# Kernel tuning notes

Hardware: AMD Instinct MI355X
Metric: run time of the kernel (lower is better)

## Reference

```python
import jax, jax.numpy as jnp
import numpy as np

DICE_TH = 0.4
CLS_TH = 0.5
LN_EPS = 1e-5


def setup_inputs() -> dict:
    key = jax.random.key(0)
    P, C, NC, K = 200_000, 256, 200, 24  # points, clicks, classes, latent prototypes
    ks = jax.random.split(key, 6)
    # structured masks: each click targets one of K prototype regions so the
    # dice/cls thresholds yield a non-degenerate grouping
    point_proto = jax.random.randint(ks[0], (P,), 0, K)
    proto_vals = jax.random.uniform(ks[1], (P,))
    click_proto = jax.random.randint(ks[2], (C,), 0, K)
    base = (point_proto[:, None] == click_proto[None, :]).astype(jnp.float32)  # [P, C]
    noise = jax.random.uniform(ks[3], (P, C))
    masks_heatmap = base * (0.6 + 0.4 * proto_vals[:, None]) + 0.02 * noise
    class_emb = jax.random.normal(ks[4], (K, NC)) * 3.0
    cls_logits = class_emb[click_proto] + 0.3 * jax.random.normal(ks[5], (C, NC))
    clicks_list = jax.random.randint(ks[0], (C,), 0, NC)  # unused (random_clicks=True)
    return {"masks_heatmap": masks_heatmap, "cls_logits": cls_logits,
            "clicks_list": clicks_list}


def _associate(masks_heatmap, cls_logits):
    """Greedy dice+cls-similarity grouping (random_clicks=True path).
    Returns labels[c] = leader click index of the group containing click c."""
    M = masks_heatmap                      # [P, C]
    C = M.shape[1]
    s = M.sum(0)                           # [C]
    # dice[i, j] = 2 * m_i . m_j / (sum(m_i) + sum(m_j))  (all pairs at once)
    dice = 2.0 * (M.T @ M) / (s[:, None] + s[None, :])
    # F.layer_norm over last dim, no affine
    mu = cls_logits.mean(-1, keepdims=True)
    var = ((cls_logits - mu) ** 2).mean(-1, keepdims=True)
    p = (cls_logits - mu) / jnp.sqrt(var + LN_EPS)
    sim = p @ p.T                          # [C, C]
    cond = (dice > DICE_TH) & (sim > CLS_TH)

    def step(carry, x):
        assigned, labels = carry
        i, row = x
        # skip if i already suppressed; take unsuppressed clicks matching row i
        take = row & (~assigned) & (~assigned[i])
        return (assigned | take, jnp.where(take, i, labels)), None

    init = (jnp.zeros((C,), bool), jnp.full((C,), -1, jnp.int32))
    (assigned, labels), _ = jax.lax.scan(
        step, init, (jnp.arange(C, dtype=jnp.int32), cond))
    return labels


def _merge(labels, masks_heatmap, cls_logits):
    """reduction='max': per-group max over member clicks. Unused group slots
    (non-leader indices) are zero-filled and flagged by group_valid."""
    C = masks_heatmap.shape[1]
    seg = jnp.where(labels >= 0, labels, C)  # route unassigned to dump segment
    counts = jax.ops.segment_sum(jnp.ones((C,), jnp.float32), seg,
                                 num_segments=C + 1)[:C]
    group_valid = counts > 0
    nm = jax.ops.segment_max(masks_heatmap.T, seg, num_segments=C + 1)[:C]  # [C, P]
    nc = jax.ops.segment_max(cls_logits, seg, num_segments=C + 1)[:C]      # [C, NC]
    new_masks = jnp.where(group_valid[:, None], nm, 0.0).T  # [P, C]
    new_cls = jnp.where(group_valid[:, None], nc, 0.0)      # [C, NC]
    return new_masks, new_cls, group_valid


def reference(masks_heatmap, cls_logits, clicks_list):
    labels = _associate(masks_heatmap, cls_logits)
    new_masks, new_cls, group_valid = _merge(labels, masks_heatmap, cls_logits)
    return labels, group_valid, new_masks, new_cls
```

## Files before the change

### kernel.cpp

```cpp
#include <hip/hip_runtime.h>
#include <cstdint>
#include <cstddef>

constexpr int P  = 200000;
constexpr int C  = 256;
constexpr int NC = 200;
#define DICE_TH 0.4f
#define CLS_TH  0.5f
#define LN_EPS  1e-5f

constexpr int KC = 1600;
constexpr int NCHUNK = 125;

constexpr size_t WS_G       = 0;
constexpr size_t WS_S       = 262144;
constexpr size_t WS_PROW    = 263168;
constexpr size_t WS_PT      = 467968;
constexpr size_t WS_COND    = 672768;
constexpr size_t WS_MSTART  = 680960;
constexpr size_t WS_MEMBERS = 682240;

typedef float floatx4 __attribute__((ext_vector_type(4)));
typedef float floatx16 __attribute__((ext_vector_type(16)));
typedef __bf16 bf16x4 __attribute__((ext_vector_type(4)));
typedef __bf16 bf16x8 __attribute__((ext_vector_type(8)));
typedef unsigned short ushort4v __attribute__((ext_vector_type(4)));
typedef unsigned short ushort8 __attribute__((ext_vector_type(8)));

constexpr int LDA = 40;

__global__ __launch_bounds__(256, 2) void gram_mfma_kernel(
    const float* __restrict__ M, float* __restrict__ G, float* __restrict__ s) {
  __shared__ unsigned short Abf[128 * LDA];
  __shared__ unsigned short Bbf[128 * LDA];
  __shared__ float scol[128];

  const int type = blockIdx.x;
  const int i0 = (type == 2) ? 128 : 0;
  const int j0 = (type == 0) ? 0 : 128;
  const bool diag = (type != 1);
  const int tid = threadIdx.x;
  const int wv = tid >> 6, lane = tid & 63;
  const int g  = tid & 31;
  const int kq = tid >> 5;
  const int k0 = blockIdx.y * KC;
  const int swz = (g & 3) << 1;

  if (tid < 128) scol[tid] = 0.f;

  floatx16 acc[4];
#pragma unroll
  for (int t = 0; t < 4; ++t)
#pragma unroll
    for (int r = 0; r < 16; ++r) acc[t][r] = 0.f;
  float ss[4] = {0.f, 0.f, 0.f, 0.f};

  const int mrow = lane & 31;
  const int kgrp = (lane >> 5) * 8;
  const int xa = ((mrow >> 2) & 3) << 1;
  const int wbase = (kq ^ swz) << 2;

  for (int step = 0; step < KC / 32; ++step) {
    const int kb = k0 + step * 32 + 4 * kq;
    {
      const float* src = M + (size_t)kb * 256 + i0 + 4 * g;
      floatx4 r0 = *reinterpret_cast<const floatx4*>(src);
      floatx4 r1 = *reinterpret_cast<const floatx4*>(src + 256);
      floatx4 r2 = *reinterpret_cast<const floatx4*>(src + 512);
      floatx4 r3 = *reinterpret_cast<const floatx4*>(src + 768);
      if (diag) {
        ss[0] += r0[0] + r1[0] + r2[0] + r3[0];
        ss[1] += r0[1] + r1[1] + r2[1] + r3[1];
        ss[2] += r0[2] + r1[2] + r2[2] + r3[2];
        ss[3] += r0[3] + r1[3] + r2[3] + r3[3];
      }
#pragma unroll
      for (int cc = 0; cc < 4; ++cc) {
        floatx4 f = {r0[cc], r1[cc], r2[cc], r3[cc]};
        bf16x4 b = __builtin_convertvector(f, bf16x4);
        *reinterpret_cast<ushort4v*>(&Abf[(4 * g + cc) * LDA + wbase]) =
            __builtin_bit_cast(ushort4v, b);
      }
    }
    if (!diag) {
      const float* src = M + (size_t)kb * 256 + j0 + 4 * g;
      floatx4 r0 = *reinterpret_cast<const floatx4*>(src);
      floatx4 r1 = *reinterpret_cast<const floatx4*>(src + 256);
      floatx4 r2 = *reinterpret_cast<const floatx4*>(src + 512);
      floatx4 r3 = *reinterpret_cast<const floatx4*>(src + 768);
#pragma unroll
      for (int cc = 0; cc < 4; ++cc) {
        floatx4 f = {r0[cc], r1[cc], r2[cc], r3[cc]};
        bf16x4 b = __builtin_convertvector(f, bf16x4);
        *reinterpret_cast<ushort4v*>(&Bbf[(4 * g + cc) * LDA + wbase]) =
            __builtin_bit_cast(ushort4v, b);
      }
    }
    __syncthreads();

    const unsigned short* Bsrc = diag ? Abf : Bbf;
#pragma unroll
    for (int sub = 0; sub < 2; ++sub) {
      const int ko = sub * 16 + kgrp;
      const int koff = (((ko >> 2) ^ xa) << 2);
      bf16x8 a = __builtin_bit_cast(
          bf16x8, *reinterpret_cast<const ushort8*>(
                      &Abf[(32 * wv + mrow) * LDA + koff]));
#pragma unroll
      for (int t = 0; t < 4; ++t) {
        bf16x8 b = __builtin_bit_cast(
            bf16x8, *reinterpret_cast<const ushort8*>(
                        &Bsrc[(32 * t + mrow) * LDA + koff]));
        acc[t] = __builtin_amdgcn_mfma_f32_32x32x16_bf16(a, b, acc[t], 0, 0, 0);
      }
    }
    __syncthreads();
  }

#pragma unroll
  for (int t = 0; t < 4; ++t) {
    const int gc = j0 + 32 * t + (lane & 31);
#pragma unroll
    for (int r = 0; r < 16; ++r) {
      const int gr = i0 + 32 * wv + (r & 3) + 8 * (r >> 2) + 4 * (lane >> 5);
      atomicAdd(&G[(size_t)gr * 256 + gc], acc[t][r]);
    }
  }
  if (diag) {
#pragma unroll
    for (int cc = 0; cc < 4; ++cc) atomicAdd(&scol[4 * g + cc], ss[cc]);
    __syncthreads();
    if (tid < 128) atomicAdd(&s[i0 + tid], scol[tid]);
  }
}

__global__ __launch_bounds__(64) void ln_kernel(const float* __restrict__ cls,
                                                float* __restrict__ p_row,
                                                float* __restrict__ pT) {
  const int c = blockIdx.x;
  const int t = threadIdx.x;
  const float* x = cls + (size_t)c * NC;
  float v0 = x[t];
  float v1 = x[t + 64];
  float v2 = (t < 72) ? x[t + 128] : 0.f;

  float sum = v0 + v1 + v2;
#pragma unroll
  for (int o = 32; o > 0; o >>= 1) sum += __shfl_xor(sum, o);
  const float mu = sum / (float)NC;

  float d0 = v0 - mu, d1 = v1 - mu, d2 = (t < 72) ? (v2 - mu) : 0.f;
  float sq = d0 * d0 + d1 * d1 + d2 * d2;
#pragma unroll
  for (int o = 32; o > 0; o >>= 1) sq += __shfl_xor(sq, o);
  const float var = sq / (float)NC;
  const float inv = 1.0f / sqrtf(var + LN_EPS);

  float p0 = d0 * inv, p1 = d1 * inv, p2 = d2 * inv;
  p_row[(size_t)c * NC + t] = p0;
  p_row[(size_t)c * NC + t + 64] = p1;
  pT[(size_t)t * C + c] = p0;
  pT[(size_t)(t + 64) * C + c] = p1;
  if (t < 72) {
    p_row[(size_t)c * NC + t + 128] = p2;
    pT[(size_t)(t + 128) * C + c] = p2;
  }
}

__global__ __launch_bounds__(256) void cond_kernel(
    const float* __restrict__ G, const float* __restrict__ s,
    const float* __restrict__ p_row, const float* __restrict__ pT,
    unsigned long long* __restrict__ condW) {
  __shared__ float pi[NC];
  const int i = blockIdx.x;
  const int j = threadIdx.x;
  if (j < NC) pi[j] = p_row[(size_t)i * NC + j];
  __syncthreads();

  const float si = s[i];
  const float sj = s[j];
  const float g = (i >= 128 && j < 128) ? G[(size_t)j * C + i]
                                        : G[(size_t)i * C + j];
  const float dice = 2.f * g / (si + sj);

  float acc = 0.f;
#pragma unroll 8
  for (int k = 0; k < NC; ++k) acc = fmaf(pi[k], pT[(size_t)k * C + j], acc);

  const bool cnd = (dice > DICE_TH) && (acc > CLS_TH);
  unsigned long long m = __ballot(cnd);
  if ((j & 63) == 0) condW[i * 4 + (j >> 6)] = m;
}

__global__ __launch_bounds__(64) void scan_kernel(
    const unsigned long long* __restrict__ condW,
    float* __restrict__ out_labels, float* __restrict__ out_valid,
    int* __restrict__ mstart, int* __restrict__ members) {
  __shared__ unsigned long long cS[C * 4];
  __shared__ int cnt[C];
  __shared__ int ms[C + 1];
  const int t = threadIdx.x;

  for (int idx = t; idx < C * 4; idx += 64) cS[idx] = condW[idx];
  for (int idx = t; idx < C; idx += 64) cnt[idx] = 0;
  __syncthreads();

  unsigned long long asg[4] = {0ull, 0ull, 0ull, 0ull};
  int lab[4] = {-1, -1, -1, -1};

#pragma unroll
  for (int w = 0; w < 4; ++w) {
    for (int b = 0; b < 64; ++b) {
      const int i = w * 64 + b;
      if (!((asg[w] >> b) & 1ull)) {
#pragma unroll
        for (int w2 = 0; w2 < 4; ++w2) {
          unsigned long long tk = cS[i * 4 + w2] & ~asg[w2];
          asg[w2] |= tk;
          if ((tk >> t) & 1ull) lab[w2] = i;
        }
      }
    }
  }

#pragma unroll
  for (int w = 0; w < 4; ++w)
    if (lab[w] >= 0) atomicAdd(&cnt[lab[w]], 1);
  __syncthreads();

  if (t == 0) {
    ms[0] = 0;
    for (int c2 = 0; c2 < C; ++c2) ms[c2 + 1] = ms[c2] + cnt[c2];
  }
  __syncthreads();
  for (int idx = t; idx < C; idx += 64) cnt[idx] = ms[idx];
  __syncthreads();
#pragma unroll
  for (int w = 0; w < 4; ++w) {
    if (lab[w] >= 0) {
      int pos = atomicAdd(&cnt[lab[w]], 1);
      members[pos] = w * 64 + t;
    }
  }
#pragma unroll
  for (int w = 0; w < 4; ++w) {
    const int col = w * 64 + t;
    out_labels[col] = (float)lab[w];
    out_valid[col] = (ms[col + 1] > ms[col]) ? 1.0f : 0.0f;
  }
  for (int idx = t; idx < C + 1; idx += 64) mstart[idx] = ms[idx];
}

__global__ __launch_bounds__(256) void merge_masks_kernel(
    const float* __restrict__ M, const int* __restrict__ mstart,
    const int* __restrict__ members, float* __restrict__ out_masks) {
  __shared__ float rows[8 * 256];
  __shared__ int msS[C + 1];
  __shared__ int memS[C];
  const int tid = threadIdx.x;
  const size_t p0 = (size_t)blockIdx.x * 8;

  msS[tid] = mstart[tid];
  if (tid == 0) msS[C] = mstart[C];
  memS[tid] = members[tid];

  const float4* src = reinterpret_cast<const float4*>(M + p0 * 256);
#pragma unroll
  for (int it = 0; it < 2; ++it)
    reinterpret_cast<float4*>(rows)[it * 256 + tid] = src[it * 256 + tid];
  __syncthreads();

  const int st = msS[tid], en = msS[tid + 1];
  float mx[8];
  if (en > st) {
    const int m0 = memS[st];
#pragma unroll
    for (int r = 0; r < 8; ++r) mx[r] = rows[r * 256 + m0];
    for (int k = st + 1; k < en; ++k) {
      const int mm = memS[k];
#pragma unroll
      for (int r = 0; r < 8; ++r) mx[r] = fmaxf(mx[r], rows[r * 256 + mm]);
    }
  } else {
#pragma unroll
    for (int r = 0; r < 8; ++r) mx[r] = 0.f;
  }
  __syncthreads();
#pragma unroll
  for (int r = 0; r < 8; ++r) rows[r * 256 + tid] = mx[r];
  __syncthreads();

  const int r2 = tid >> 6;
  const int cg = (tid & 63) << 2;
#pragma unroll
  for (int pass = 0; pass < 2; ++pass) {
    const int rr = pass * 4 + r2;
    floatx4 v = *reinterpret_cast<const floatx4*>(&rows[rr * 256 + cg]);
    __builtin_nontemporal_store(
        v, reinterpret_cast<floatx4*>(&out_masks[(p0 + rr) * 256 + cg]));
  }
}

__global__ __launch_bounds__(256) void merge_cls_kernel(
    const float* __restrict__ cls, const int* __restrict__ mstart,
    const int* __restrict__ members, float* __restrict__ out_cls) {
  __shared__ int se[2];
  const int c = blockIdx.x;
  const int t = threadIdx.x;
  if (t < 2) se[t] = mstart[c + t];
  __syncthreads();
  const int st = se[0], en = se[1];
  if (t < NC) {
    float mx = 0.f;
    if (en > st) {
      mx = cls[(size_t)members[st] * NC + t];
      for (int k = st + 1; k < en; ++k)
        mx = fmaxf(mx, cls[(size_t)members[k] * NC + t]);
    }
    out_cls[(size_t)c * NC + t] = mx;
  }
}

extern "C" void kernel_launch(void* const* d_in, const int* in_sizes, int n_in,
                              void* d_out, int out_size, void* d_ws,
                              size_t ws_size, hipStream_t stream) {
  const float* M = (const float*)d_in[0];
  const float* cls = (const float*)d_in[1];

  float* out = (float*)d_out;
  char* ws = (char*)d_ws;
  float* G = (float*)(ws + WS_G);
  float* s = (float*)(ws + WS_S);
  float* p_row = (float*)(ws + WS_PROW);
  float* pT = (float*)(ws + WS_PT);
  unsigned long long* condW = (unsigned long long*)(ws + WS_COND);
  int* mstart = (int*)(ws + WS_MSTART);
  int* members = (int*)(ws + WS_MEMBERS);

  float* out_labels = out;
  float* out_valid = out + 256;
  float* out_masks = out + 512;
  float* out_cls = out + 512 + (size_t)P * 256;

  hipMemsetAsync(ws, 0, WS_S + 1024, stream);

  gram_mfma_kernel<<<dim3(3, NCHUNK), 256, 0, stream>>>(M, G, s);
  ln_kernel<<<C, 64, 0, stream>>>(cls, p_row, pT);
  cond_kernel<<<C, 256, 0, stream>>>(G, s, p_row, pT, condW);
  scan_kernel<<<1, 64, 0, stream>>>(condW, out_labels, out_valid, mstart,
                                    members);
  merge_masks_kernel<<<P / 8, 256, 0, stream>>>(M, mstart, members, out_masks);
  merge_cls_kernel<<<C, 256, 0, stream>>>(cls, mstart, members, out_cls);
}
```

Measured before the change: 430.4 us.

## Prefetch next K-step into registers, use 2x2 wave tiling, and reduce partials deterministically

The gram kernel now loads the next 32-row K slice into registers while the MFMAs for the current slice run, which overlaps global loads with compute. Waves are arranged as a 2x2 grid of 64x64 tiles, so each wave reads two A and two B fragments instead of one A and four B, cutting LDS reads. When the workspace is large enough, each chunk writes its partial 128x128 tile to a scratch buffer and a separate reduce kernel sums the partials. This replaces roughly 6M float atomics, at the cost of about 24MB of extra scratch writes and reads plus one more kernel launch.

New measurement: 417.6 us. 1.03x faster.

```diff
diff --git a/kernel.cpp b/kernel.cpp
--- a/kernel.cpp
+++ b/kernel.cpp
@@ -11,6 +11,7 @@
 
 constexpr int KC = 1600;
 constexpr int NCHUNK = 125;
+constexpr int NSTEP = KC / 32;
 
 constexpr size_t WS_G       = 0;
 constexpr size_t WS_S       = 262144;
@@ -19,6 +20,8 @@
 constexpr size_t WS_COND    = 672768;
 constexpr size_t WS_MSTART  = 680960;
 constexpr size_t WS_MEMBERS = 682240;
+constexpr size_t WS_PART    = 1048576;
+constexpr size_t PART_BYTES = (size_t)NCHUNK * 3 * 16384 * 4;
 
 typedef float floatx4 __attribute__((ext_vector_type(4)));
 typedef float floatx16 __attribute__((ext_vector_type(16)));
@@ -30,7 +33,8 @@
 constexpr int LDA = 40;
 
 __global__ __launch_bounds__(256, 2) void gram_mfma_kernel(
-    const float* __restrict__ M, float* __restrict__ G, float* __restrict__ s) {
+    const float* __restrict__ M, float* __restrict__ G, float* __restrict__ s,
+    float* __restrict__ part) {
   __shared__ unsigned short Abf[128 * LDA];
   __shared__ unsigned short Bbf[128 * LDA];
   __shared__ float scol[128];
@@ -41,10 +45,11 @@
   const bool diag = (type != 1);
   const int tid = threadIdx.x;
   const int wv = tid >> 6, lane = tid & 63;
+  const int wr = wv >> 1, wc = wv & 1;
   const int g  = tid & 31;
   const int kq = tid >> 5;
-  const int k0 = blockIdx.y * KC;
-  const int swz = (g & 3) << 1;
+  const int chunk = blockIdx.y;
+  const int k0 = chunk * KC;
 
   if (tid < 128) scol[tid] = 0.f;
 
@@ -58,73 +63,116 @@
   const int mrow = lane & 31;
   const int kgrp = (lane >> 5) * 8;
   const int xa = ((mrow >> 2) & 3) << 1;
-  const int wbase = (kq ^ swz) << 2;
-
-  for (int step = 0; step < KC / 32; ++step) {
-    const int kb = k0 + step * 32 + 4 * kq;
-    {
-      const float* src = M + (size_t)kb * 256 + i0 + 4 * g;
-      floatx4 r0 = *reinterpret_cast<const floatx4*>(src);
-      floatx4 r1 = *reinterpret_cast<const floatx4*>(src + 256);
-      floatx4 r2 = *reinterpret_cast<const floatx4*>(src + 512);
-      floatx4 r3 = *reinterpret_cast<const floatx4*>(src + 768);
-      if (diag) {
-        ss[0] += r0[0] + r1[0] + r2[0] + r3[0];
-        ss[1] += r0[1] + r1[1] + r2[1] + r3[1];
-        ss[2] += r0[2] + r1[2] + r2[2] + r3[2];
-        ss[3] += r0[3] + r1[3] + r2[3] + r3[3];
-      }
-#pragma unroll
-      for (int cc = 0; cc < 4; ++cc) {
-        floatx4 f = {r0[cc], r1[cc], r2[cc], r3[cc]};
-        bf16x4 b = __builtin_convertvector(f, bf16x4);
-        *reinterpret_cast<ushort4v*>(&Abf[(4 * g + cc) * LDA + wbase]) =
-            __builtin_bit_cast(ushort4v, b);
-      }
+  const int wbase = (kq ^ ((g & 3) << 1)) << 2;
+
+  const float* baseA = M + i0 + 4 * g;
+  const float* baseB = M + j0 + 4 * g;
+
+#define LOADS(dst, base, step_)                                              \
+  {                                                                          \
+    const float* src_ = (base) + (size_t)(k0 + (step_) * 32 + 4 * kq) * 256; \
+    dst[0] = *reinterpret_cast<const floatx4*>(src_);                        \
+    dst[1] = *reinterpret_cast<const floatx4*>(src_ + 256);                  \
+    dst[2] = *reinterpret_cast<const floatx4*>(src_ + 512);                  \
+    dst[3] = *reinterpret_cast<const floatx4*>(src_ + 768);                  \
+  }
+
+#define STAGE(dstLds, r_)                                                    \
+  {                                                                          \
+    _Pragma("unroll") for (int cc = 0; cc < 4; ++cc) {                       \
+      floatx4 f = {r_[0][cc], r_[1][cc], r_[2][cc], r_[3][cc]};              \
+      bf16x4 b = __builtin_convertvector(f, bf16x4);                         \
+      *reinterpret_cast<ushort4v*>(&dstLds[(4 * g + cc) * LDA + wbase]) =    \
+          __builtin_bit_cast(ushort4v, b);                                   \
+    }                                                                        \
+  }
+
+#define SSUM(r_)                                                             \
+  if (diag) {                                                                \
+    ss[0] += r_[0][0] + r_[1][0] + r_[2][0] + r_[3][0];                      \
+    ss[1] += r_[0][1] + r_[1][1] + r_[2][1] + r_[3][1];                      \
+    ss[2] += r_[0][2] + r_[1][2] + r_[2][2] + r_[3][2];                      \
+    ss[3] += r_[0][3] + r_[1][3] + r_[2][3] + r_[3][3];                      \
+  }
+
+#define MFMA_STEP()                                                          \
+  {                                                                          \
+    const unsigned short* Bsrc = diag ? Abf : Bbf;                           \
+    _Pragma("unroll") for (int sub = 0; sub < 2; ++sub) {                    \
+      const int ko = sub * 16 + kgrp;                                        \
+      const int koff = (((ko >> 2) ^ xa) << 2);                              \
+      bf16x8 av0 = __builtin_bit_cast(                                       \
+          bf16x8, *reinterpret_cast<const ushort8*>(                         \
+                      &Abf[(64 * wr + mrow) * LDA + koff]));                 \
+      bf16x8 av1 = __builtin_bit_cast(                                       \
+          bf16x8, *reinterpret_cast<const ushort8*>(                         \
+                      &Abf[(64 * wr + 32 + mrow) * LDA + koff]));            \
+      bf16x8 bv0 = __builtin_bit_cast(                                       \
+          bf16x8, *reinterpret_cast<const ushort8*>(                         \
+                      &Bsrc[(64 * wc + mrow) * LDA + koff]));                \
+      bf16x8 bv1 = __builtin_bit_cast(                                       \
+          bf16x8, *reinterpret_cast<const ushort8*>(                         \
+                      &Bsrc[(64 * wc + 32 + mrow) * LDA + koff]));           \
+      acc[0] = __builtin_amdgcn_mfma_f32_32x32x16_bf16(av0, bv0, acc[0], 0, 0, 0); \
+      acc[1] = __builtin_amdgcn_mfma_f32_32x32x16_bf16(av0, bv1, acc[1], 0, 0, 0); \
+      acc[2] = __builtin_amdgcn_mfma_f32_32x32x16_bf16(av1, bv0, acc[2], 0, 0, 0); \
+      acc[3] = __builtin_amdgcn_mfma_f32_32x32x16_bf16(av1, bv1, acc[3], 0, 0, 0); \
+    }                                                                        \
+  }
+
+  floatx4 a0[4], a1[4], b0[4], b1[4];
+  LOADS(a0, baseA, 0);
+  if (!diag) LOADS(b0, baseB, 0);
+
+  for (int sp = 0; sp < NSTEP; sp += 2) {
+    SSUM(a0);
+    STAGE(Abf, a0);
+    if (!diag) STAGE(Bbf, b0);
+    __syncthreads();
+    LOADS(a1, baseA, sp + 1);
+    if (!diag) LOADS(b1, baseB, sp + 1);
+    MFMA_STEP();
+    __syncthreads();
+
+    SSUM(a1);
+    STAGE(Abf, a1);
+    if (!diag) STAGE(Bbf, b1);
+    __syncthreads();
+    if (sp + 2 < NSTEP) {
+      LOADS(a0, baseA, sp + 2);
+      if (!diag) LOADS(b0, baseB, sp + 2);
     }
-    if (!diag) {
-      const float* src = M + (size_t)kb * 256 + j0 + 4 * g;
-      floatx4 r0 = *reinterpret_cast<const floatx4*>(src);
-      floatx4 r1 = *reinterpret_cast<const floatx4*>(src + 256);
-      floatx4 r2 = *reinterpret_cast<const floatx4*>(src + 512);
-      floatx4 r3 = *reinterpret_cast<const floatx4*>(src + 768);
-#pragma unroll
-      for (int cc = 0; cc < 4; ++cc) {
-        floatx4 f = {r0[cc], r1[cc], r2[cc], r3[cc]};
-        bf16x4 b = __builtin_convertvector(f, bf16x4);
-        *reinterpret_cast<ushort4v*>(&Bbf[(4 * g + cc) * LDA + wbase]) =
-            __builtin_bit_cast(ushort4v, b);
-      }
-    }
+    MFMA_STEP();
     __syncthreads();
-
-    const unsigned short* Bsrc = diag ? Abf : Bbf;
-#pragma unroll
-    for (int sub = 0; sub < 2; ++sub) {
-      const int ko = sub * 16 + kgrp;
-      const int koff = (((ko >> 2) ^ xa) << 2);
-      bf16x8 a = __builtin_bit_cast(
-          bf16x8, *reinterpret_cast<const ushort8*>(
-                      &Abf[(32 * wv + mrow) * LDA + koff]));
-#pragma unroll
-      for (int t = 0; t < 4; ++t) {
-        bf16x8 b = __builtin_bit_cast(
-            bf16x8, *reinterpret_cast<const ushort8*>(
-                        &Bsrc[(32 * t + mrow) * LDA + koff]));
-        acc[t] = __builtin_amdgcn_mfma_f32_32x32x16_bf16(a, b, acc[t], 0, 0, 0);
-      }
-    }
-    __syncthreads();
-  }
-
-#pragma unroll
-  for (int t = 0; t < 4; ++t) {
-    const int gc = j0 + 32 * t + (lane & 31);
-#pragma unroll
-    for (int r = 0; r < 16; ++r) {
-      const int gr = i0 + 32 * wv + (r & 3) + 8 * (r >> 2) + 4 * (lane >> 5);
-      atomicAdd(&G[(size_t)gr * 256 + gc], acc[t][r]);
-    }
+  }
+#undef LOADS
+#undef STAGE
+#undef SSUM
+#undef MFMA_STEP
+
+  if (part != nullptr) {
+    float* Pp = part + ((size_t)chunk * 3 + type) * 16384;
+#pragma unroll
+    for (int ai = 0; ai < 2; ++ai)
+#pragma unroll
+      for (int bj = 0; bj < 2; ++bj)
+#pragma unroll
+        for (int r = 0; r < 16; ++r) {
+          const int lr = 64 * wr + 32 * ai + (r & 3) + 8 * (r >> 2) + 4 * (lane >> 5);
+          const int lc = 64 * wc + 32 * bj + (lane & 31);
+          Pp[lr * 128 + lc] = acc[ai * 2 + bj][r];
+        }
+  } else {
+#pragma unroll
+    for (int ai = 0; ai < 2; ++ai)
+#pragma unroll
+      for (int bj = 0; bj < 2; ++bj)
+#pragma unroll
+        for (int r = 0; r < 16; ++r) {
+          const int gr = i0 + 64 * wr + 32 * ai + (r & 3) + 8 * (r >> 2) + 4 * (lane >> 5);
+          const int gc = j0 + 64 * wc + 32 * bj + (lane & 31);
+          atomicAdd(&G[(size_t)gr * 256 + gc], acc[ai * 2 + bj][r]);
+        }
   }
   if (diag) {
 #pragma unroll
@@ -132,6 +180,27 @@
     __syncthreads();
     if (tid < 128) atomicAdd(&s[i0 + tid], scol[tid]);
   }
+}
+
+__global__ __launch_bounds__(128) void reduce_g_kernel(
+    const float* __restrict__ part, float* __restrict__ G) {
+  const int slot = blockIdx.x >> 7;
+  const int lr = blockIdx.x & 127;
+  const int lc = threadIdx.x;
+  const float* src = part + (size_t)slot * 16384 + (size_t)lr * 128 + lc;
+  float s0 = 0.f, s1 = 0.f, s2 = 0.f, s3 = 0.f, s4 = 0.f;
+  int ch = 0;
+  for (; ch + 5 <= NCHUNK; ch += 5) {
+    s0 += src[(size_t)(ch + 0) * 49152];
+    s1 += src[(size_t)(ch + 1) * 49152];
+    s2 += src[(size_t)(ch + 2) * 49152];
+    s3 += src[(size_t)(ch + 3) * 49152];
+    s4 += src[(size_t)(ch + 4) * 49152];
+  }
+  for (; ch < NCHUNK; ++ch) s0 += src[(size_t)ch * 49152];
+  const int i0 = (slot == 2) ? 128 : 0;
+  const int j0 = (slot == 0) ? 0 : 128;
+  G[(size_t)(i0 + lr) * 256 + (j0 + lc)] = ((s0 + s1) + (s2 + s3)) + s4;
 }
 
 __global__ __launch_bounds__(64) void ln_kernel(const float* __restrict__ cls,
@@ -342,9 +411,17 @@
   float* out_masks = out + 512;
   float* out_cls = out + 512 + (size_t)P * 256;
 
-  hipMemsetAsync(ws, 0, WS_S + 1024, stream);
-
-  gram_mfma_kernel<<<dim3(3, NCHUNK), 256, 0, stream>>>(M, G, s);
+  const bool bigws = ws_size >= WS_PART + PART_BYTES;
+  float* part = bigws ? (float*)(ws + WS_PART) : nullptr;
+
+  if (bigws) {
+    hipMemsetAsync(ws + WS_S, 0, 1024, stream);
+  } else {
+    hipMemsetAsync(ws, 0, WS_S + 1024, stream);
+  }
+
+  gram_mfma_kernel<<<dim3(3, NCHUNK), 256, 0, stream>>>(M, G, s, part);
+  if (bigws) reduce_g_kernel<<<384, 128, 0, stream>>>(part, G);
   ln_kernel<<<C, 64, 0, stream>>>(cls, p_row, pT);
   cond_kernel<<<C, 256, 0, stream>>>(G, s, p_row, pT, condW);
   scan_kernel<<<1, 64, 0, stream>>>(condW, out_labels, out_valid, mstart,
```
